# Performance work log

Measured on AMD Instinct MI355X. Metric: run time of the kernel, lower is better.

Reference implementation:

```python
import jax, jax.numpy as jnp
import numpy as np

N_NODES = 20000
N_EDGES = 320000
C = 64  # classes
NEG_SLOPE = 0.2  # DGL GATConv default


def setup_inputs() -> dict:
    key = jax.random.key(0)
    ks = jax.random.split(key, 32)
    dims = [C, 2 * C, 4 * C, 8 * C, 16 * C]
    inp = {}
    inp["feat"] = jax.random.normal(ks[0], (N_NODES, C), jnp.float32)
    k = 1
    for i in range(4):
        din, dout = dims[i], dims[i + 1]
        scale = 1.0 / np.sqrt(din)
        inp[f"W{i+1}"] = jax.random.normal(ks[k], (din, dout), jnp.float32) * scale; k += 1
        inp[f"al{i+1}"] = jax.random.normal(ks[k], (dout,), jnp.float32) * 0.1; k += 1
        inp[f"ar{i+1}"] = jax.random.normal(ks[k], (dout,), jnp.float32) * 0.1; k += 1
        inp[f"b{i+1}"] = jnp.zeros((dout,), jnp.float32)
    inp["relW"] = jax.random.normal(ks[k], (16 * C, C), jnp.float32) * (1.0 / np.sqrt(16 * C)); k += 1
    inp["relB"] = jnp.zeros((C,), jnp.float32)
    inp["src"] = jax.random.randint(ks[k], (N_EDGES,), 0, N_NODES, jnp.int32); k += 1
    inp["dst"] = jax.random.randint(ks[k], (N_EDGES,), 0, N_NODES, jnp.int32); k += 1
    inp["rel"] = jnp.ones((C,), jnp.int32)
    inp["order"] = 1023
    return inp


def _gat_layer(x, W, al, ar, b, src, dst, n_nodes):
    """DGL GATConv (num_heads=1, allow_zero_in_degree=True, activation=tanh)."""
    h = x @ W                                   # [N, D] projected features
    el = h @ al                                 # [N] attn_l score per node
    er = h @ ar                                 # [N] attn_r score per node
    e = jax.nn.leaky_relu(el[src] + er[dst], NEG_SLOPE)          # [E]
    # segment (edge) softmax over incoming edges of each dst node
    m = jax.ops.segment_max(e, dst, num_segments=n_nodes)        # [N]
    ex = jnp.exp(e - m[dst])                                      # [E]
    s = jax.ops.segment_sum(ex, dst, num_segments=n_nodes)       # [N]
    alpha = ex / s[dst]                                           # [E]
    # gather neighbor messages, weight by attention, scatter-add to dst
    out = jax.ops.segment_sum(h[src] * alpha[:, None], dst, num_segments=n_nodes)  # [N, D]
    return jnp.tanh(out + b)


def reference(feat, W1, al1, ar1, b1, W2, al2, ar2, b2, W3, al3, ar3, b3,
              W4, al4, ar4, b4, relW, relB, src, dst, rel, order):
    n = feat.shape[0]
    h = _gat_layer(feat, W1, al1, ar1, b1, src, dst, n)
    h = _gat_layer(h, W2, al2, ar2, b2, src, dst, n)
    h = _gat_layer(h, W3, al3, ar3, b3, src, dst, n)
    h = _gat_layer(h, W4, al4, ar4, b4, src, dst, n)
    embeddings = h[: order + 1]                  # first order+1 node embeddings
    pooling = jnp.mean(embeddings, axis=0)       # [16C]
    logits = pooling @ relW + relB               # [C]
    nz = jnp.nonzero(rel, size=rel.shape[0])[0]  # static-size nonzero (rel is all-ones)
    return logits[nz]
```

## Files before the change

kernel.cpp:

```cpp
#include <hip/hip_runtime.h>
#include <hip/hip_bf16.h>

#define NN 20000
#define NE 320000
#define MPAD 20096
#define ORD 1024
#define NB 79

typedef __hip_bfloat16 bf16;
typedef __attribute__((ext_vector_type(8))) short bf16x8;
typedef __attribute__((ext_vector_type(4))) float f32x4;

static __device__ __forceinline__ float b2f(bf16 x) { return __bfloat162float(x); }
static __device__ __forceinline__ float bfbits2f(short s) {
    unsigned int u = ((unsigned int)(unsigned short)s) << 16;
    float f; __builtin_memcpy(&f, &u, 4); return f;
}
static __device__ __forceinline__ short f2bfbits(float v) {
    bf16 h = __float2bfloat16(v);
    short s; __builtin_memcpy(&s, &h, 2); return s;
}
static __device__ __forceinline__ unsigned short f2bfu(float v) {
    bf16 h = __float2bfloat16(v);
    unsigned short s; __builtin_memcpy(&s, &h, 2); return s;
}

__global__ void setup_all(const float* __restrict__ feat,
                          const float* __restrict__ W1, const float* __restrict__ al1, const float* __restrict__ ar1,
                          const float* __restrict__ W2, const float* __restrict__ al2, const float* __restrict__ ar2,
                          const float* __restrict__ W3, const float* __restrict__ al3, const float* __restrict__ ar3,
                          const float* __restrict__ W4, const float* __restrict__ al4, const float* __restrict__ ar4,
                          bf16* __restrict__ featb, bf16* __restrict__ wt1,
                          bf16* __restrict__ wt2, bf16* __restrict__ wt3,
                          bf16* __restrict__ wt4, int* __restrict__ counts,
                          int* __restrict__ hglob,
                          float* __restrict__ walbuf, float* __restrict__ warbuf) {
    int b = blockIdx.x;
    if (b < 960) {
        const float *W, *al, *ar; int dout, k; float *wal, *war;
        if (b < 64)       { W = W1; al = al1; ar = ar1; dout = 128;  k = b;       wal = walbuf;        war = warbuf; }
        else if (b < 192) { W = W2; al = al2; ar = ar2; dout = 256;  k = b - 64;  wal = walbuf + 512;  war = warbuf + 512; }
        else if (b < 448) { W = W3; al = al3; ar = ar3; dout = 512;  k = b - 192; wal = walbuf + 1024; war = warbuf + 1024; }
        else              { W = W4; al = al4; ar = ar4; dout = 1024; k = b - 448; wal = walbuf + 1536; war = warbuf + 1536; }
        const float* row = W + (long)k * dout;
        float sl = 0.f, sr = 0.f;
        for (int j = threadIdx.x; j < dout; j += 256) {
            float w = row[j];
            sl += w * al[j];
            sr += w * ar[j];
        }
        __shared__ float sbl[256], sbr[256];
        sbl[threadIdx.x] = sl; sbr[threadIdx.x] = sr;
        __syncthreads();
        for (int st = 128; st > 0; st >>= 1) {
            if (threadIdx.x < st) {
                sbl[threadIdx.x] += sbl[threadIdx.x + st];
                sbr[threadIdx.x] += sbr[threadIdx.x + st];
            }
            __syncthreads();
        }
        if (threadIdx.x == 0) { wal[k] = sbl[0]; war[k] = sbr[0]; }
        return;
    }
    int i = (b - 960) * 256 + threadIdx.x;
    if (i < NN) counts[i] = 0;
    if (i < 256) hglob[i] = 0;
    if (i < 1280000) { featb[i] = __float2bfloat16(feat[i]); return; }
    i -= 1280000;
    if (i < 8192)  { int r = i >> 7,  c = i & 127;  wt1[c * 64 + r]  = __float2bfloat16(W1[i]); return; }
    i -= 8192;
    if (i < 32768) { int r = i >> 8,  c = i & 255;  wt2[c * 128 + r] = __float2bfloat16(W2[i]); return; }
    i -= 32768;
    if (i < 131072){ int r = i >> 9,  c = i & 511;  wt3[c * 256 + r] = __float2bfloat16(W3[i]); return; }
    i -= 131072;
    if (i < 524288){ int r = i >> 10, c = i & 1023; wt4[c * 512 + r] = __float2bfloat16(W4[i]); return; }
}

__global__ void hist_kernel(const int* __restrict__ dst, int* __restrict__ counts, int n) {
    int i = blockIdx.x * blockDim.x + threadIdx.x;
    if (i < n) atomicAdd(&counts[dst[i]], 1);
}

__global__ void csr_phase1(const int* __restrict__ counts, int* __restrict__ blocksums,
                           int* __restrict__ hglob) {
    __shared__ int sb[256];
    __shared__ int hh[256];
    int tid = threadIdx.x;
    hh[tid] = 0;
    int i = blockIdx.x * 256 + tid;
    int c = (i < NN) ? counts[i] : 0;
    sb[tid] = c;
    __syncthreads();
    for (int st = 128; st > 0; st >>= 1) {
        if (tid < st) sb[tid] += sb[tid + st];
        __syncthreads();
    }
    if (tid == 0) blocksums[blockIdx.x] = sb[0];
    if (i < NN) {
        int d = c > 255 ? 255 : c;
        atomicAdd(&hh[d], 1);
    }
    __syncthreads();
    if (hh[tid] > 0) atomicAdd(&hglob[tid], hh[tid]);
}

__global__ void csr_phase2(const int* __restrict__ counts, const int* __restrict__ blocksums,
                           int* __restrict__ offsets, int* __restrict__ cursor,
                           const int* __restrict__ hglob, int* __restrict__ curg) {
    int tid = threadIdx.x;
    if (blockIdx.x == NB) {
        __shared__ int hs[256];
        int orig = hglob[tid];
        hs[tid] = orig;
        __syncthreads();
        for (int st = 1; st < 256; st <<= 1) {
            int u = (tid >= st) ? hs[tid - st] : 0;
            __syncthreads();
            hs[tid] += u;
            __syncthreads();
        }
        curg[tid] = hs[tid] - orig;
        return;
    }
    __shared__ int bs[256];
    bs[tid] = (tid < NB) ? blocksums[tid] : 0;
    __syncthreads();
    for (int st = 1; st < 256; st <<= 1) {
        int u = (tid >= st) ? bs[tid - st] : 0;
        __syncthreads();
        bs[tid] += u;
        __syncthreads();
    }
    int base = (blockIdx.x == 0) ? 0 : bs[blockIdx.x - 1];
    __shared__ int sc[256];
    int i = blockIdx.x * 256 + tid;
    int c = (i < NN) ? counts[i] : 0;
    sc[tid] = c;
    __syncthreads();
    for (int st = 1; st < 256; st <<= 1) {
        int u = (tid >= st) ? sc[tid - st] : 0;
        __syncthreads();
        sc[tid] += u;
        __syncthreads();
    }
    int excl = base + sc[tid] - c;
    if (i < NN) { offsets[i] = excl; cursor[i] = excl; }
    if (i == NN - 1) offsets[NN] = excl + c;
}

__global__ void scatter_elr(const int* __restrict__ src, const int* __restrict__ dst,
                            int* __restrict__ cursor, int* __restrict__ esrc,
                            const int* __restrict__ counts, int* __restrict__ curg,
                            int* __restrict__ nodeperm,
                            const bf16* __restrict__ X, const float* __restrict__ wal,
                            const float* __restrict__ war, float* __restrict__ el,
                            float* __restrict__ er) {
    int b = blockIdx.x;
    if (b < 1250) {
        int i = b * 256 + threadIdx.x;
        int p = atomicAdd(&cursor[dst[i]], 1);
        esrc[p] = src[i];
        return;
    }
    if (b < 1250 + NB) {
        __shared__ int hh[256];
        __shared__ int basep[256];
        int tid = threadIdx.x;
        hh[tid] = 0;
        __syncthreads();
        int i = (b - 1250) * 256 + tid;
        int d = 0, rank = 0;
        bool valid = (i < NN);
        if (valid) {
            d = counts[i]; if (d > 255) d = 255;
            rank = atomicAdd(&hh[d], 1);
        }
        __syncthreads();
        if (hh[tid] > 0) basep[tid] = atomicAdd(&curg[tid], hh[tid]);
        __syncthreads();
        if (valid) nodeperm[basep[d] + rank] = i;
        return;
    }
    int idx = (b - 1250 - NB) * 256 + threadIdx.x;
    int node = idx >> 6;
    int lane = threadIdx.x & 63;
    if (node >= NN) return;
    float x = bfbits2f(*((const short*)X + (long)node * 64 + lane));
    float sl = x * wal[lane];
    float sr = x * war[lane];
    #pragma unroll
    for (int o = 32; o > 0; o >>= 1) {
        sl += __shfl_down(sl, o);
        sr += __shfl_down(sr, o);
    }
    if (lane == 0) { el[node] = sl; er[node] = sr; }
}

__global__ void edge_softmax_w(const int* __restrict__ off, const int* __restrict__ esrc,
                               const float* __restrict__ el, const float* __restrict__ er,
                               float* __restrict__ alpha, int n) {
    int node = blockIdx.x * 4 + (threadIdx.x >> 6);
    if (node >= n) return;
    int lane = threadIdx.x & 63;
    int s = off[node], e = off[node + 1];
    int deg = e - s;
    if (deg <= 0) return;
    float erd = er[node];
    if (deg <= 64) {
        float v = -1e30f;
        if (lane < deg) {
            float t = el[esrc[s + lane]] + erd;
            v = t >= 0.f ? t : 0.2f * t;
        }
        float mx = v;
        #pragma unroll
        for (int o = 32; o > 0; o >>= 1) mx = fmaxf(mx, __shfl_xor(mx, o));
        float x = (lane < deg) ? __expf(v - mx) : 0.f;
        float ssum = x;
        #pragma unroll
        for (int o = 32; o > 0; o >>= 1) ssum += __shfl_xor(ssum, o);
        if (lane < deg) alpha[s + lane] = x / ssum;
    } else if (deg <= 256) {
        float v[4];
        float mx = -1e30f;
        #pragma unroll
        for (int r = 0; r < 4; r++) {
            v[r] = -1e30f;
            if (r * 64 + lane < deg) {
                float t = el[esrc[s + r * 64 + lane]] + erd;
                v[r] = t >= 0.f ? t : 0.2f * t;
            }
            mx = fmaxf(mx, v[r]);
        }
        #pragma unroll
        for (int o = 32; o > 0; o >>= 1) mx = fmaxf(mx, __shfl_xor(mx, o));
        float ssum = 0.f;
        #pragma unroll
        for (int r = 0; r < 4; r++) {
            v[r] = (r * 64 + lane < deg) ? __expf(v[r] - mx) : 0.f;
            ssum += v[r];
        }
        #pragma unroll
        for (int o = 32; o > 0; o >>= 1) ssum += __shfl_xor(ssum, o);
        float inv = 1.f / ssum;
        #pragma unroll
        for (int r = 0; r < 4; r++)
            if (r * 64 + lane < deg) alpha[s + r * 64 + lane] = v[r] * inv;
    } else if (lane == 0) {
        float mx = -1e30f;
        for (int j = s; j < e; j++) {
            float t = el[esrc[j]] + erd;
            t = t >= 0.f ? t : 0.2f * t;
            alpha[j] = t;
            mx = fmaxf(mx, t);
        }
        float ssum = 0.f;
        for (int j = s; j < e; j++) { float x = __expf(alpha[j] - mx); alpha[j] = x; ssum += x; }
        float inv = 1.f / ssum;
        for (int j = s; j < e; j++) alpha[j] *= inv;
    }
}

__global__ void aggregate_e(const bf16* __restrict__ X, const float* __restrict__ alpha,
                            const int* __restrict__ esrc, const int* __restrict__ off,
                            const int* __restrict__ perm, float* __restrict__ zbuf, int zn,
                            bf16* __restrict__ Y, int din, int log2chunks, int nmax) {
    {
        int z = blockIdx.x * 256 + threadIdx.x;
        if (z < zn) zbuf[z] = 0.f;
    }
    int chunk = blockIdx.x & ((1 << log2chunks) - 1);
    int nb = blockIdx.x >> log2chunks;
    int sub = threadIdx.x >> 3, sl = threadIdx.x & 7;
    int slot = nb * 32 + sub;
    if (slot >= nmax) return;
    int node = perm ? perm[slot] : slot;
    const short* xb = (const short*)X + chunk * 64 + sl * 8;
    float acc[8] = {0.f,0.f,0.f,0.f,0.f,0.f,0.f,0.f};
    int s = off[node], e = off[node + 1];
    int j = s;
    for (; j + 8 <= e; j += 8) {
        float a[8]; int r[8]; bf16x8 w[8];
        #pragma unroll
        for (int q = 0; q < 8; q++) { a[q] = alpha[j + q]; r[q] = esrc[j + q]; }
        #pragma unroll
        for (int q = 0; q < 8; q++) w[q] = *(const bf16x8*)(xb + (long)r[q] * din);
        #pragma unroll
        for (int q = 0; q < 8; q++)
            #pragma unroll
            for (int v = 0; v < 8; v++) acc[v] += a[q] * bfbits2f(w[q][v]);
    }
    for (; j + 4 <= e; j += 4) {
        float a0 = alpha[j],     a1 = alpha[j + 1];
        float a2 = alpha[j + 2], a3 = alpha[j + 3];
        int r0 = esrc[j],     r1 = esrc[j + 1];
        int r2 = esrc[j + 2], r3 = esrc[j + 3];
        bf16x8 w0 = *(const bf16x8*)(xb + (long)r0 * din);
        bf16x8 w1 = *(const bf16x8*)(xb + (long)r1 * din);
        bf16x8 w2 = *(const bf16x8*)(xb + (long)r2 * din);
        bf16x8 w3 = *(const bf16x8*)(xb + (long)r3 * din);
        #pragma unroll
        for (int v = 0; v < 8; v++) acc[v] += a0 * bfbits2f(w0[v]);
        #pragma unroll
        for (int v = 0; v < 8; v++) acc[v] += a1 * bfbits2f(w1[v]);
        #pragma unroll
        for (int v = 0; v < 8; v++) acc[v] += a2 * bfbits2f(w2[v]);
        #pragma unroll
        for (int v = 0; v < 8; v++) acc[v] += a3 * bfbits2f(w3[v]);
    }
    for (; j < e; j++) {
        float a = alpha[j];
        bf16x8 w = *(const bf16x8*)(xb + (long)esrc[j] * din);
        #pragma unroll
        for (int v = 0; v < 8; v++) acc[v] += a * bfbits2f(w[v]);
    }
    short outv[8];
    #pragma unroll
    for (int v = 0; v < 8; v++) outv[v] = f2bfbits(acc[v]);
    bf16x8 store;
    __builtin_memcpy(&store, outv, sizeof(store));
    *(bf16x8*)((short*)Y + (long)node * din + chunk * 64 + sl * 8) = store;
}

__global__ __launch_bounds__(256, 4)
void gemm_k64(const bf16* __restrict__ A, const bf16* __restrict__ WT,
              const float* __restrict__ bias, bf16* __restrict__ C,
              const float* __restrict__ wal, const float* __restrict__ war,
              float* __restrict__ elp, float* __restrict__ erp) {
    int gw = blockIdx.x * 4 + (threadIdx.x >> 6);
    if (gw >= 2500) return;
    int r0 = (gw >> 1) << 4;
    int col0 = (gw & 1) << 6;
    int lane = threadIdx.x & 63;
    int m = lane & 15, quad = lane >> 4;

    const short* Ab = (const short*)A + (long)(r0 + m) * 64 + quad * 8;
    bf16x8 a0 = *(const bf16x8*)(Ab);
    bf16x8 a1 = *(const bf16x8*)(Ab + 32);

    f32x4 acc[4];
    bf16x8 b0[4], b1[4];
    #pragma unroll
    for (int t = 0; t < 4; t++) {
        acc[t] = (f32x4){0.f, 0.f, 0.f, 0.f};
        const short* Bb = (const short*)WT + (long)(col0 + t * 16 + m) * 64 + quad * 8;
        b0[t] = *(const bf16x8*)(Bb);
        b1[t] = *(const bf16x8*)(Bb + 32);
    }
    #pragma unroll
    for (int t = 0; t < 4; t++) {
        acc[t] = __builtin_amdgcn_mfma_f32_16x16x32_bf16(a0, b0[t], acc[t], 0, 0, 0);
        acc[t] = __builtin_amdgcn_mfma_f32_16x16x32_bf16(a1, b1[t], acc[t], 0, 0, 0);
    }

    float sl4[4] = {0.f, 0.f, 0.f, 0.f};
    float sr4[4] = {0.f, 0.f, 0.f, 0.f};
    #pragma unroll
    for (int t = 0; t < 4; t++) {
        int col = col0 + t * 16 + m;
        float bb = bias[col];
        float wl = wal[col], wrr = war[col];
        #pragma unroll
        for (int r = 0; r < 4; r++) {
            float v = tanhf(acc[t][r] + bb);
            sl4[r] += v * wl;
            sr4[r] += v * wrr;
            float vn = __shfl_xor(v, 1);
            if ((m & 1) == 0) {
                unsigned int pk = (unsigned int)f2bfu(v) | ((unsigned int)f2bfu(vn) << 16);
                int row = r0 + quad * 4 + r;
                *(unsigned int*)((short*)C + (long)row * 128 + col) = pk;
            }
        }
    }
    #pragma unroll
    for (int r = 0; r < 4; r++) {
        float s1 = sl4[r], s2 = sr4[r];
        #pragma unroll
        for (int o = 1; o < 16; o <<= 1) {
            s1 += __shfl_xor(s1, o);
            s2 += __shfl_xor(s2, o);
        }
        if (m == 0) {
            int row = r0 + quad * 4 + r;
            atomicAdd(&elp[row], s1);
            atomicAdd(&erp[row], s2);
        }
    }
}

__global__ __launch_bounds__(256, 4)
void gemm_tiled(const bf16* __restrict__ A, const bf16* __restrict__ WT,
                const float* __restrict__ bias, bf16* __restrict__ C,
                const float* __restrict__ wal, const float* __restrict__ war,
                float* __restrict__ elp, float* __restrict__ erp,
                int M, int K, int N, int ncols, int nrows) {
    __shared__ short smem[16384];
    short* As = smem;
    short* Bs = smem + 8192;
    int g = blockIdx.x;
    int rowTile = ((g >> 3) / ncols) * 8 + (g & 7);
    int colTile = (g >> 3) % ncols;
    if (rowTile >= nrows) return;
    int row0 = rowTile << 7, col0 = colTile << 7;
    int tid = threadIdx.x;
    int lane = tid & 63, wave = tid >> 6;
    int wr = (wave >> 1) << 6;
    int wc = (wave & 1) << 6;
    int m = lane & 15, quad = lane >> 4;

    f32x4 acc[4][4];
    #pragma unroll
    for (int i = 0; i < 4; i++)
        #pragma unroll
        for (int j = 0; j < 4; j++) acc[i][j] = (f32x4){0.f, 0.f, 0.f, 0.f};

    const short* Ab = (const short*)A;
    const short* Bb = (const short*)WT;
    long ga[4], gb[4];
    #pragma unroll
    for (int n = 0; n < 4; n++) {
        int chunk = n * 256 + tid;
        int row = chunk >> 3;
        int qg = (chunk & 7) ^ (row & 7);
        ga[n] = (long)(row0 + row) * K + qg * 8;
        gb[n] = (long)(col0 + row) * K + qg * 8;
    }

    typedef const __attribute__((address_space(1))) void cgvoid;
    typedef __attribute__((address_space(3))) void lvoid;

    for (int k0 = 0; k0 < K; k0 += 64) {
        __syncthreads();
        #pragma unroll
        for (int n = 0; n < 4; n++)
            __builtin_amdgcn_global_load_lds((cgvoid*)(Ab + ga[n] + k0),
                                             (lvoid*)(As + (n * 256 + tid) * 8), 16, 0, 0);
        #pragma unroll
        for (int n = 0; n < 4; n++)
            __builtin_amdgcn_global_load_lds((cgvoid*)(Bb + gb[n] + k0),
                                             (lvoid*)(Bs + (n * 256 + tid) * 8), 16, 0, 0);
        __syncthreads();
        #pragma unroll
        for (int h = 0; h < 2; h++) {
            bf16x8 af[4], bfr[4];
            #pragma unroll
            for (int s = 0; s < 4; s++) {
                int ra = wr + s * 16 + m;
                int sa = (h * 4 + quad) ^ (ra & 7);
                af[s] = *(const bf16x8*)(As + ra * 64 + sa * 8);
                int rb = wc + s * 16 + m;
                int sb = (h * 4 + quad) ^ (rb & 7);
                bfr[s] = *(const bf16x8*)(Bs + rb * 64 + sb * 8);
            }
            #pragma unroll
            for (int i = 0; i < 4; i++)
                #pragma unroll
                for (int j = 0; j < 4; j++)
                    acc[i][j] = __builtin_amdgcn_mfma_f32_16x16x32_bf16(af[i], bfr[j], acc[i][j], 0, 0, 0);
        }
    }

    float bb[4], walr[4], warr[4];
    #pragma unroll
    for (int j = 0; j < 4; j++) {
        int col = col0 + wc + j * 16 + m;
        bb[j] = bias[col];
        if (elp) { walr[j] = wal[col]; warr[j] = war[col]; }
    }
    __syncthreads();
    short* myep = smem + wave * 1152;
    #pragma unroll
    for (int i = 0; i < 4; i++) {
        float sl4[4] = {0.f, 0.f, 0.f, 0.f};
        float sr4[4] = {0.f, 0.f, 0.f, 0.f};
        #pragma unroll
        for (int j = 0; j < 4; j++) {
            #pragma unroll
            for (int r = 0; r < 4; r++) {
                float v = tanhf(acc[i][j][r] + bb[j]);
                if (elp) { sl4[r] += v * walr[j]; sr4[r] += v * warr[j]; }
                float vn = __shfl_xor(v, 1);
                if ((m & 1) == 0) {
                    unsigned int pk = (unsigned int)f2bfu(v) | ((unsigned int)f2bfu(vn) << 16);
                    *(unsigned int*)(myep + (quad * 4 + r) * 72 + j * 16 + m) = pk;
                }
            }
        }
        #pragma unroll
        for (int pass = 0; pass < 2; pass++) {
            int lr = pass * 8 + (lane >> 3);
            int lc = (lane & 7) * 8;
            bf16x8 v = *(const bf16x8*)(myep + lr * 72 + lc);
            int row = row0 + wr + i * 16 + lr;
            if (row < M)
                *(bf16x8*)((short*)C + (long)row * N + col0 + wc + lc) = v;
        }
        if (elp) {
            #pragma unroll
            for (int r = 0; r < 4; r++) {
                float s1 = sl4[r], s2 = sr4[r];
                #pragma unroll
                for (int o = 1; o < 16; o <<= 1) {
                    s1 += __shfl_xor(s1, o);
                    s2 += __shfl_xor(s2, o);
                }
                if (m == 0) {
                    int row = row0 + wr + i * 16 + quad * 4 + r;
                    if (row < M) {
                        atomicAdd(&elp[row], s1);
                        atomicAdd(&erp[row], s2);
                    }
                }
            }
        }
    }
}

__global__ void pool_sum(const bf16* __restrict__ X, const int* __restrict__ order,
                         float* __restrict__ poolsum) {
    int cg = blockIdx.x & 3, rs = blockIdx.x >> 2;
    int c = cg * 256 + threadIdx.x;
    int rows = order[0] + 1;
    float s = 0.f;
    for (int r = rs; r < rows; r += 64) s += b2f(X[(long)r * 1024 + c]);
    atomicAdd(&poolsum[c], s);
}

__global__ void head_logits(const float* __restrict__ poolsum, const float* __restrict__ relW,
                            const float* __restrict__ relB, const int* __restrict__ order,
                            float* __restrict__ logits) {
    int t = blockIdx.x;
    float s = 0.f;
    for (int c = threadIdx.x; c < 1024; c += 256)
        s += poolsum[c] * relW[(long)c * 64 + t];
    __shared__ float sb[256];
    sb[threadIdx.x] = s;
    __syncthreads();
    for (int st = 128; st > 0; st >>= 1) {
        if (threadIdx.x < st) sb[threadIdx.x] += sb[threadIdx.x + st];
        __syncthreads();
    }
    if (threadIdx.x == 0) {
        float rows = (float)(order[0] + 1);
        logits[t] = sb[0] / rows + relB[t];
    }
}

__global__ void head_gather(const float* __restrict__ logits, const int* __restrict__ rel,
                            float* __restrict__ out) {
    __shared__ int nzv[64];
    int t = threadIdx.x;
    if (t == 0) {
        int k = 0;
        for (int i = 0; i < 64; i++)
            if (rel[i] != 0) nzv[k++] = i;
        for (; k < 64; k++) nzv[k] = 0;
    }
    __syncthreads();
    out[t] = logits[nzv[t]];
}

extern "C" void kernel_launch(void* const* d_in, const int* in_sizes, int n_in,
                              void* d_out, int out_size, void* d_ws, size_t ws_size,
                              hipStream_t stream) {
    const float* feat = (const float*)d_in[0];
    const float* W[4]  = {(const float*)d_in[1], (const float*)d_in[5], (const float*)d_in[9],  (const float*)d_in[13]};
    const float* al[4] = {(const float*)d_in[2], (const float*)d_in[6], (const float*)d_in[10], (const float*)d_in[14]};
    const float* ar[4] = {(const float*)d_in[3], (const float*)d_in[7], (const float*)d_in[11], (const float*)d_in[15]};
    const float* bias[4] = {(const float*)d_in[4], (const float*)d_in[8], (const float*)d_in[12], (const float*)d_in[16]};
    const float* relW = (const float*)d_in[17];
    const float* relB = (const float*)d_in[18];
    const int* src = (const int*)d_in[19];
    const int* dst = (const int*)d_in[20];
    const int* rel = (const int*)d_in[21];
    const int* order = (const int*)d_in[22];

    const int dims[5] = {64, 128, 256, 512, 1024};

    char* p = (char*)d_ws;
    auto carve = [&](size_t bytes) {
        void* r = (void*)p;
        p += (bytes + 255) & ~(size_t)255;
        return r;
    };
    bf16* xbuf = (bf16*)carve((size_t)MPAD * 1024 * sizeof(bf16));
    bf16* ybuf = (bf16*)carve((size_t)MPAD * 512 * sizeof(bf16));
    bf16* featb = (bf16*)carve((size_t)MPAD * 64 * sizeof(bf16));
    bf16* wt[4];
    for (int l = 0; l < 4; l++)
        wt[l] = (bf16*)carve((size_t)dims[l] * dims[l + 1] * sizeof(bf16));
    float* walbuf = (float*)carve(4 * 512 * sizeof(float));
    float* warbuf = (float*)carve(4 * 512 * sizeof(float));
    float* elbuf[2];
    elbuf[0] = (float*)carve((size_t)2 * NN * sizeof(float));
    elbuf[1] = (float*)carve((size_t)2 * NN * sizeof(float));
    float* alpha = (float*)carve((size_t)NE * sizeof(float));
    int* counts  = (int*)carve((size_t)NN * sizeof(int));
    int* offsets = (int*)carve((size_t)(NN + 1) * sizeof(int));
    int* cursor  = (int*)carve((size_t)NN * sizeof(int));
    int* esrc    = (int*)carve((size_t)NE * sizeof(int));
    int* nodeperm = (int*)carve((size_t)NN * sizeof(int));
    int* blocksums = (int*)carve((size_t)NB * sizeof(int));
    int* hglob   = (int*)carve(256 * sizeof(int));
    int* curg    = (int*)carve(256 * sizeof(int));
    float* poolsum = (float*)carve(1024 * sizeof(float));
    float* logits  = (float*)carve(64 * sizeof(float));

    setup_all<<<960 + 7720, 256, 0, stream>>>(
        feat, W[0], al[0], ar[0], W[1], al[1], ar[1],
        W[2], al[2], ar[2], W[3], al[3], ar[3],
        featb, wt[0], wt[1], wt[2], wt[3], counts, hglob, walbuf, warbuf);

    hist_kernel<<<(NE + 255) / 256, 256, 0, stream>>>(dst, counts, NE);
    csr_phase1<<<NB, 256, 0, stream>>>(counts, blocksums, hglob);
    csr_phase2<<<NB + 1, 256, 0, stream>>>(counts, blocksums, offsets, cursor, hglob, curg);
    scatter_elr<<<1250 + NB + 5000, 256, 0, stream>>>(src, dst, cursor, esrc,
                                                      counts, curg, nodeperm,
                                                      featb, walbuf, warbuf,
                                                      elbuf[0], elbuf[0] + NN);

    const bf16* x = featb;
    const int nrows = MPAD / 128;
    const int nrowsPad = 160;
    const int log2c[4] = {0, 1, 2, 3};
    for (int l = 0; l < 4; l++) {
        int K = dims[l], N = dims[l + 1];
        float* elr_rd = elbuf[l & 1];
        float* elr_wr = elbuf[(l + 1) & 1];
        int nsm   = (l < 3) ? NN : ORD;
        int nmax  = (l < 3) ? NN : ORD;
        int nodeBlocks = (nmax + 31) / 32;
        const int* aggPerm = (l < 3) ? nodeperm : nullptr;
        edge_softmax_w<<<(nsm + 3) / 4, 256, 0, stream>>>(offsets, esrc, elr_rd,
                                                          elr_rd + NN, alpha, nsm);
        float* zbuf = (l < 3) ? elr_wr : poolsum;
        int zn = (l < 3) ? 2 * NN : 1024;
        aggregate_e<<<nodeBlocks << log2c[l], 256, 0, stream>>>(
            x, alpha, esrc, offsets, aggPerm, zbuf, zn, ybuf, K, log2c[l], nmax);
        int ncols = N >> 7;
        if (l == 0) {
            gemm_k64<<<625, 256, 0, stream>>>(ybuf, wt[0], bias[0], xbuf,
                                              walbuf + 512, warbuf + 512,
                                              elr_wr, elr_wr + NN);
        } else if (l < 3) {
            gemm_tiled<<<nrowsPad * ncols, 256, 0, stream>>>(
                ybuf, wt[l], bias[l], xbuf,
                walbuf + (l + 1) * 512, warbuf + (l + 1) * 512,
                elr_wr, elr_wr + NN,
                NN, K, N, ncols, nrows);
        } else {
            gemm_tiled<<<8 * ncols, 256, 0, stream>>>(
                ybuf, wt[l], bias[l], xbuf,
                nullptr, nullptr, nullptr, nullptr,
                ORD, K, N, ncols, 8);
        }
        x = xbuf;
    }

    pool_sum<<<256, 256, 0, stream>>>(xbuf, order, poolsum);
    head_logits<<<64, 256, 0, stream>>>(poolsum, relW, relB, order, logits);
    head_gather<<<1, 64, 0, stream>>>(logits, rel, (float*)d_out);
}
```

Before: 303.0 us.

## Fuse edge softmax into aggregation and merge head kernels into one

The separate edge-softmax kernel is removed. Each 8-thread group in the aggregation kernel now computes its destination node's softmax itself, keeping the weights in LDS for degree up to 64 and recomputing them on the fly for larger degrees, so the alpha buffer is never written to or read from global memory. The three head kernels (pool sum, logits, gather) become one kernel that folds the mean pooling into the relW dot product and uses a last-block atomic counter to compact the nonzero outputs. The trade-offs are that the softmax is recomputed for every feature chunk, and every head block rereads the full 1024-row embedding tile instead of reading one pooled vector.

```diff
diff --git a/kernel.cpp b/kernel.cpp
--- a/kernel.cpp
+++ b/kernel.cpp
@@ -196,75 +196,12 @@
     if (lane == 0) { el[node] = sl; er[node] = sr; }
 }
 
-__global__ void edge_softmax_w(const int* __restrict__ off, const int* __restrict__ esrc,
-                               const float* __restrict__ el, const float* __restrict__ er,
-                               float* __restrict__ alpha, int n) {
-    int node = blockIdx.x * 4 + (threadIdx.x >> 6);
-    if (node >= n) return;
-    int lane = threadIdx.x & 63;
-    int s = off[node], e = off[node + 1];
-    int deg = e - s;
-    if (deg <= 0) return;
-    float erd = er[node];
-    if (deg <= 64) {
-        float v = -1e30f;
-        if (lane < deg) {
-            float t = el[esrc[s + lane]] + erd;
-            v = t >= 0.f ? t : 0.2f * t;
-        }
-        float mx = v;
-        #pragma unroll
-        for (int o = 32; o > 0; o >>= 1) mx = fmaxf(mx, __shfl_xor(mx, o));
-        float x = (lane < deg) ? __expf(v - mx) : 0.f;
-        float ssum = x;
-        #pragma unroll
-        for (int o = 32; o > 0; o >>= 1) ssum += __shfl_xor(ssum, o);
-        if (lane < deg) alpha[s + lane] = x / ssum;
-    } else if (deg <= 256) {
-        float v[4];
-        float mx = -1e30f;
-        #pragma unroll
-        for (int r = 0; r < 4; r++) {
-            v[r] = -1e30f;
-            if (r * 64 + lane < deg) {
-                float t = el[esrc[s + r * 64 + lane]] + erd;
-                v[r] = t >= 0.f ? t : 0.2f * t;
-            }
-            mx = fmaxf(mx, v[r]);
-        }
-        #pragma unroll
-        for (int o = 32; o > 0; o >>= 1) mx = fmaxf(mx, __shfl_xor(mx, o));
-        float ssum = 0.f;
-        #pragma unroll
-        for (int r = 0; r < 4; r++) {
-            v[r] = (r * 64 + lane < deg) ? __expf(v[r] - mx) : 0.f;
-            ssum += v[r];
-        }
-        #pragma unroll
-        for (int o = 32; o > 0; o >>= 1) ssum += __shfl_xor(ssum, o);
-        float inv = 1.f / ssum;
-        #pragma unroll
-        for (int r = 0; r < 4; r++)
-            if (r * 64 + lane < deg) alpha[s + r * 64 + lane] = v[r] * inv;
-    } else if (lane == 0) {
-        float mx = -1e30f;
-        for (int j = s; j < e; j++) {
-            float t = el[esrc[j]] + erd;
-            t = t >= 0.f ? t : 0.2f * t;
-            alpha[j] = t;
-            mx = fmaxf(mx, t);
-        }
-        float ssum = 0.f;
-        for (int j = s; j < e; j++) { float x = __expf(alpha[j] - mx); alpha[j] = x; ssum += x; }
-        float inv = 1.f / ssum;
-        for (int j = s; j < e; j++) alpha[j] *= inv;
-    }
-}
-
-__global__ void aggregate_e(const bf16* __restrict__ X, const float* __restrict__ alpha,
-                            const int* __restrict__ esrc, const int* __restrict__ off,
-                            const int* __restrict__ perm, float* __restrict__ zbuf, int zn,
-                            bf16* __restrict__ Y, int din, int log2chunks, int nmax) {
+__global__ void aggregate_sm(const bf16* __restrict__ X,
+                             const float* __restrict__ el, const float* __restrict__ er,
+                             const int* __restrict__ esrc, const int* __restrict__ off,
+                             const int* __restrict__ perm, float* __restrict__ zbuf, int zn,
+                             bf16* __restrict__ Y, int din, int log2chunks, int nmax) {
+    __shared__ __attribute__((aligned(16))) float alds[32][68];
     {
         int z = blockIdx.x * 256 + threadIdx.x;
         if (z < zn) zbuf[z] = 0.f;
@@ -275,44 +212,127 @@
     int slot = nb * 32 + sub;
     if (slot >= nmax) return;
     int node = perm ? perm[slot] : slot;
+    int s = off[node], e = off[node + 1];
+    int deg = e - s;
+    bool fast = (deg <= 64);
+
+    float erd = (deg > 0) ? er[node] : 0.f;
+    float vmax = -1e30f, inv = 0.f;
+    if (fast) {
+        float v[8];
+        #pragma unroll
+        for (int t = 0; t < 8; t++) {
+            v[t] = -1e30f;
+            int idx = sl + 8 * t;
+            if (idx < deg) {
+                float x = el[esrc[s + idx]] + erd;
+                v[t] = x >= 0.f ? x : 0.2f * x;
+            }
+            vmax = fmaxf(vmax, v[t]);
+        }
+        #pragma unroll
+        for (int o = 1; o < 8; o <<= 1) vmax = fmaxf(vmax, __shfl_xor(vmax, o));
+        float ssum = 0.f;
+        #pragma unroll
+        for (int t = 0; t < 8; t++) {
+            int idx = sl + 8 * t;
+            if (idx < deg) { v[t] = __expf(v[t] - vmax); ssum += v[t]; }
+        }
+        #pragma unroll
+        for (int o = 1; o < 8; o <<= 1) ssum += __shfl_xor(ssum, o);
+        inv = 1.f / ssum;
+        #pragma unroll
+        for (int t = 0; t < 8; t++) {
+            int idx = sl + 8 * t;
+            if (idx < deg) alds[sub][idx] = v[t] * inv;
+        }
+    } else {
+        for (int j = s + sl; j < e; j += 8) {
+            float x = el[esrc[j]] + erd;
+            x = x >= 0.f ? x : 0.2f * x;
+            vmax = fmaxf(vmax, x);
+        }
+        #pragma unroll
+        for (int o = 1; o < 8; o <<= 1) vmax = fmaxf(vmax, __shfl_xor(vmax, o));
+        float ssum = 0.f;
+        for (int j = s + sl; j < e; j += 8) {
+            float x = el[esrc[j]] + erd;
+            x = x >= 0.f ? x : 0.2f * x;
+            ssum += __expf(x - vmax);
+        }
+        #pragma unroll
+        for (int o = 1; o < 8; o <<= 1) ssum += __shfl_xor(ssum, o);
+        inv = 1.f / ssum;
+    }
+
     const short* xb = (const short*)X + chunk * 64 + sl * 8;
     float acc[8] = {0.f,0.f,0.f,0.f,0.f,0.f,0.f,0.f};
-    int s = off[node], e = off[node + 1];
     int j = s;
-    for (; j + 8 <= e; j += 8) {
-        float a[8]; int r[8]; bf16x8 w[8];
-        #pragma unroll
-        for (int q = 0; q < 8; q++) { a[q] = alpha[j + q]; r[q] = esrc[j + q]; }
-        #pragma unroll
-        for (int q = 0; q < 8; q++) w[q] = *(const bf16x8*)(xb + (long)r[q] * din);
-        #pragma unroll
-        for (int q = 0; q < 8; q++)
-            #pragma unroll
-            for (int v = 0; v < 8; v++) acc[v] += a[q] * bfbits2f(w[q][v]);
-    }
-    for (; j + 4 <= e; j += 4) {
-        float a0 = alpha[j],     a1 = alpha[j + 1];
-        float a2 = alpha[j + 2], a3 = alpha[j + 3];
-        int r0 = esrc[j],     r1 = esrc[j + 1];
-        int r2 = esrc[j + 2], r3 = esrc[j + 3];
-        bf16x8 w0 = *(const bf16x8*)(xb + (long)r0 * din);
-        bf16x8 w1 = *(const bf16x8*)(xb + (long)r1 * din);
-        bf16x8 w2 = *(const bf16x8*)(xb + (long)r2 * din);
-        bf16x8 w3 = *(const bf16x8*)(xb + (long)r3 * din);
-        #pragma unroll
-        for (int v = 0; v < 8; v++) acc[v] += a0 * bfbits2f(w0[v]);
-        #pragma unroll
-        for (int v = 0; v < 8; v++) acc[v] += a1 * bfbits2f(w1[v]);
-        #pragma unroll
-        for (int v = 0; v < 8; v++) acc[v] += a2 * bfbits2f(w2[v]);
-        #pragma unroll
-        for (int v = 0; v < 8; v++) acc[v] += a3 * bfbits2f(w3[v]);
-    }
-    for (; j < e; j++) {
-        float a = alpha[j];
-        bf16x8 w = *(const bf16x8*)(xb + (long)esrc[j] * din);
-        #pragma unroll
-        for (int v = 0; v < 8; v++) acc[v] += a * bfbits2f(w[v]);
+    if (fast) {
+        for (; j + 8 <= e; j += 8) {
+            int ofs = j - s;
+            f32x4 a0 = *(const f32x4*)&alds[sub][ofs];
+            f32x4 a1 = *(const f32x4*)&alds[sub][ofs + 4];
+            int r[8]; bf16x8 w[8];
+            #pragma unroll
+            for (int q = 0; q < 8; q++) r[q] = esrc[j + q];
+            #pragma unroll
+            for (int q = 0; q < 8; q++) w[q] = *(const bf16x8*)(xb + (long)r[q] * din);
+            #pragma unroll
+            for (int q = 0; q < 4; q++)
+                #pragma unroll
+                for (int v = 0; v < 8; v++) acc[v] += a0[q] * bfbits2f(w[q][v]);
+            #pragma unroll
+            for (int q = 0; q < 4; q++)
+                #pragma unroll
+                for (int v = 0; v < 8; v++) acc[v] += a1[q] * bfbits2f(w[4 + q][v]);
+        }
+        for (; j + 4 <= e; j += 4) {
+            int ofs = j - s;
+            f32x4 a0 = *(const f32x4*)&alds[sub][ofs];
+            int r[4]; bf16x8 w[4];
+            #pragma unroll
+            for (int q = 0; q < 4; q++) r[q] = esrc[j + q];
+            #pragma unroll
+            for (int q = 0; q < 4; q++) w[q] = *(const bf16x8*)(xb + (long)r[q] * din);
+            #pragma unroll
+            for (int q = 0; q < 4; q++)
+                #pragma unroll
+                for (int v = 0; v < 8; v++) acc[v] += a0[q] * bfbits2f(w[q][v]);
+        }
+        for (; j < e; j++) {
+            float a = alds[sub][j - s];
+            bf16x8 w = *(const bf16x8*)(xb + (long)esrc[j] * din);
+            #pragma unroll
+            for (int v = 0; v < 8; v++) acc[v] += a * bfbits2f(w[v]);
+        }
+    } else {
+        for (; j + 8 <= e; j += 8) {
+            int r[8]; float a[8]; bf16x8 w[8];
+            #pragma unroll
+            for (int q = 0; q < 8; q++) r[q] = esrc[j + q];
+            #pragma unroll
+            for (int q = 0; q < 8; q++) {
+                float x = el[r[q]] + erd;
+                x = x >= 0.f ? x : 0.2f * x;
+                a[q] = __expf(x - vmax) * inv;
+            }
+            #pragma unroll
+            for (int q = 0; q < 8; q++) w[q] = *(const bf16x8*)(xb + (long)r[q] * din);
+            #pragma unroll
+            for (int q = 0; q < 8; q++)
+                #pragma unroll
+                for (int v = 0; v < 8; v++) acc[v] += a[q] * bfbits2f(w[q][v]);
+        }
+        for (; j < e; j++) {
+            int r = esrc[j];
+            float x = el[r] + erd;
+            x = x >= 0.f ? x : 0.2f * x;
+            float a = __expf(x - vmax) * inv;
+            bf16x8 w = *(const bf16x8*)(xb + (long)r * din);
+            #pragma unroll
+            for (int v = 0; v < 8; v++) acc[v] += a * bfbits2f(w[v]);
+        }
     }
     short outv[8];
     #pragma unroll
@@ -517,48 +537,58 @@
     }
 }
 
-__global__ void pool_sum(const bf16* __restrict__ X, const int* __restrict__ order,
-                         float* __restrict__ poolsum) {
-    int cg = blockIdx.x & 3, rs = blockIdx.x >> 2;
-    int c = cg * 256 + threadIdx.x;
+__global__ void head_all(const bf16* __restrict__ X, const float* __restrict__ relW,
+                         const float* __restrict__ relB, const int* __restrict__ order,
+                         const int* __restrict__ rel, float* __restrict__ logits,
+                         float* __restrict__ out) {
+    int t = blockIdx.x;
     int rows = order[0] + 1;
+    int wave = threadIdx.x >> 6, lane = threadIdx.x & 63;
+
+    float wreg0[8], wreg1[8];
+    #pragma unroll
+    for (int v = 0; v < 8; v++) wreg0[v] = relW[(long)(lane * 16 + v) * 64 + t];
+    #pragma unroll
+    for (int v = 0; v < 8; v++) wreg1[v] = relW[(long)(lane * 16 + 8 + v) * 64 + t];
+
     float s = 0.f;
-    for (int r = rs; r < rows; r += 64) s += b2f(X[(long)r * 1024 + c]);
-    atomicAdd(&poolsum[c], s);
-}
-
-__global__ void head_logits(const float* __restrict__ poolsum, const float* __restrict__ relW,
-                            const float* __restrict__ relB, const int* __restrict__ order,
-                            float* __restrict__ logits) {
-    int t = blockIdx.x;
-    float s = 0.f;
-    for (int c = threadIdx.x; c < 1024; c += 256)
-        s += poolsum[c] * relW[(long)c * 64 + t];
-    __shared__ float sb[256];
-    sb[threadIdx.x] = s;
+    for (int r = wave; r < rows; r += 4) {
+        const short* xr = (const short*)X + (long)r * 1024 + lane * 16;
+        bf16x8 x0 = *(const bf16x8*)xr;
+        bf16x8 x1 = *(const bf16x8*)(xr + 8);
+        #pragma unroll
+        for (int v = 0; v < 8; v++) s += bfbits2f(x0[v]) * wreg0[v];
+        #pragma unroll
+        for (int v = 0; v < 8; v++) s += bfbits2f(x1[v]) * wreg1[v];
+    }
+    #pragma unroll
+    for (int o = 32; o > 0; o >>= 1) s += __shfl_xor(s, o);
+
+    __shared__ float wsum[4];
+    __shared__ int lastf;
+    if (lane == 0) wsum[wave] = s;
     __syncthreads();
-    for (int st = 128; st > 0; st >>= 1) {
-        if (threadIdx.x < st) sb[threadIdx.x] += sb[threadIdx.x + st];
-        __syncthreads();
-    }
     if (threadIdx.x == 0) {
-        float rows = (float)(order[0] + 1);
-        logits[t] = sb[0] / rows + relB[t];
-    }
-}
-
-__global__ void head_gather(const float* __restrict__ logits, const int* __restrict__ rel,
-                            float* __restrict__ out) {
-    __shared__ int nzv[64];
-    int t = threadIdx.x;
-    if (t == 0) {
-        int k = 0;
-        for (int i = 0; i < 64; i++)
-            if (rel[i] != 0) nzv[k++] = i;
-        for (; k < 64; k++) nzv[k] = 0;
+        float tot = wsum[0] + wsum[1] + wsum[2] + wsum[3];
+        float val = tot / (float)rows + relB[t];
+        atomicAdd(&logits[t], val);
+        __threadfence();
+        unsigned int old = atomicAdd((unsigned int*)(logits + 64), 1u);
+        lastf = (old == 63u) ? 1 : 0;
     }
     __syncthreads();
-    out[t] = logits[nzv[t]];
+    if (lastf && threadIdx.x < 64) {
+        int li = threadIdx.x;
+        __threadfence();
+        float lv = atomicAdd(&logits[li], 0.f);
+        int rv = rel[li];
+        unsigned long long mask = __ballot(rv != 0);
+        int pos = __popcll(mask & ((1ULL << li) - 1));
+        int count = __popcll(mask);
+        float l0 = __shfl(lv, 0);
+        if (rv) out[pos] = lv;
+        if (li >= count) out[li] = l0;
+    }
 }
 
 extern "C" void kernel_launch(void* const* d_in, const int* in_sizes, int n_in,
@@ -595,7 +625,6 @@
     float* elbuf[2];
     elbuf[0] = (float*)carve((size_t)2 * NN * sizeof(float));
     elbuf[1] = (float*)carve((size_t)2 * NN * sizeof(float));
-    float* alpha = (float*)carve((size_t)NE * sizeof(float));
     int* counts  = (int*)carve((size_t)NN * sizeof(int));
     int* offsets = (int*)carve((size_t)(NN + 1) * sizeof(int));
     int* cursor  = (int*)carve((size_t)NN * sizeof(int));
@@ -605,7 +634,6 @@
     int* hglob   = (int*)carve(256 * sizeof(int));
     int* curg    = (int*)carve(256 * sizeof(int));
     float* poolsum = (float*)carve(1024 * sizeof(float));
-    float* logits  = (float*)carve(64 * sizeof(float));
 
     setup_all<<<960 + 7720, 256, 0, stream>>>(
         feat, W[0], al[0], ar[0], W[1], al[1], ar[1],
@@ -628,16 +656,13 @@
         int K = dims[l], N = dims[l + 1];
         float* elr_rd = elbuf[l & 1];
         float* elr_wr = elbuf[(l + 1) & 1];
-        int nsm   = (l < 3) ? NN : ORD;
         int nmax  = (l < 3) ? NN : ORD;
         int nodeBlocks = (nmax + 31) / 32;
         const int* aggPerm = (l < 3) ? nodeperm : nullptr;
-        edge_softmax_w<<<(nsm + 3) / 4, 256, 0, stream>>>(offsets, esrc, elr_rd,
-                                                          elr_rd + NN, alpha, nsm);
         float* zbuf = (l < 3) ? elr_wr : poolsum;
         int zn = (l < 3) ? 2 * NN : 1024;
-        aggregate_e<<<nodeBlocks << log2c[l], 256, 0, stream>>>(
-            x, alpha, esrc, offsets, aggPerm, zbuf, zn, ybuf, K, log2c[l], nmax);
+        aggregate_sm<<<nodeBlocks << log2c[l], 256, 0, stream>>>(
+            x, elr_rd, elr_rd + NN, esrc, offsets, aggPerm, zbuf, zn, ybuf, K, log2c[l], nmax);
         int ncols = N >> 7;
         if (l == 0) {
             gemm_k64<<<625, 256, 0, stream>>>(ybuf, wt[0], bias[0], xbuf,
@@ -658,7 +683,5 @@
         x = xbuf;
     }
 
-    pool_sum<<<256, 256, 0, stream>>>(xbuf, order, poolsum);
-    head_logits<<<64, 256, 0, stream>>>(poolsum, relW, relB, order, logits);
-    head_gather<<<1, 64, 0, stream>>>(logits, rel, (float*)d_out);
-}
+    head_all<<<64, 256, 0, stream>>>(xbuf, relW, relB, order, rel, poolsum, (float*)d_out);
+}
```

New measurement: 361.7 us. +19.4%, slower.
